# Optimization experiments

Measured on AMD Instinct MI355X. Metric: run time of the kernel, lower is better.

Reference implementation:

```python
import jax, jax.numpy as jnp
import numpy as np

B, S, D, H = 4, 2048, 1024, 16
DH = D // H


def setup_inputs() -> dict:
    key = jax.random.key(0)
    ks = jax.random.split(key, 12)
    std = 0.02
    return {
        "inputs": jax.random.normal(ks[0], (B, S, D), jnp.float32),
        "pre_block": jax.random.normal(ks[1], (B, S, D), jnp.float32),
        "ln_gamma": jnp.ones((D,), jnp.float32),
        "ln_beta": jnp.zeros((D,), jnp.float32),
        "Wq": jax.random.normal(ks[2], (D, D), jnp.float32) * std,
        "bq": jnp.zeros((D,), jnp.float32),
        "Wk": jax.random.normal(ks[3], (D, D), jnp.float32) * std,
        "bk": jnp.zeros((D,), jnp.float32),
        "Wv": jax.random.normal(ks[4], (D, D), jnp.float32) * std,
        "bv": jnp.zeros((D,), jnp.float32),
        "Wpos": jax.random.normal(ks[5], (D, D), jnp.float32) * std,
        "u_bias": jax.random.normal(ks[6], (H, DH), jnp.float32) * std,
        "v_bias": jax.random.normal(ks[7], (H, DH), jnp.float32) * std,
        "Wo": jax.random.normal(ks[8], (D, D), jnp.float32) * std,
        "bo": jnp.zeros((D,), jnp.float32),
    }


def _sinusoidal_pe(seq_len, d_model, dtype):
    pos = jnp.arange(seq_len, dtype=dtype)[:, None]                 # [S,1]
    i = jnp.arange(0, d_model, 2, dtype=dtype)
    div = jnp.exp(-(jnp.log(jnp.asarray(10000.0, dtype)) * i / d_model))  # [D/2]
    ang = pos * div                                                  # [S,D/2]
    pe = jnp.zeros((seq_len, d_model), dtype)
    pe = pe.at[:, 0::2].set(jnp.sin(ang)).at[:, 1::2].set(jnp.cos(ang))
    return pe


def _rel_shift(pos_score):
    # Transformer-XL style relative shift: pos_score [B,H,S,S]
    b, h, s1, s2 = pos_score.shape
    pad = jnp.zeros((b, h, s1, 1), pos_score.dtype)
    padded = jnp.concatenate([pad, pos_score], axis=-1)              # [B,H,S,S+1]
    padded = padded.reshape(b, h, s2 + 1, s1)
    return padded[:, :, 1:].reshape(b, h, s1, s2)


def _layer_norm(x, gamma, beta, eps=1e-5):
    mu = jnp.mean(x, axis=-1, keepdims=True)
    var = jnp.mean(jnp.square(x - mu), axis=-1, keepdims=True)
    return (x - mu) * jax.lax.rsqrt(var + eps) * gamma + beta


def reference(inputs, pre_block, ln_gamma, ln_beta, Wq, bq, Wk, bk, Wv, bv,
              Wpos, u_bias, v_bias, Wo, bo):
    b, s, d = inputs.shape
    h = u_bias.shape[0]
    dh = d // h

    pe = _sinusoidal_pe(s, d, inputs.dtype)                          # [S,D]
    x = _layer_norm(inputs, ln_gamma, ln_beta)

    q = (x @ Wq + bq).reshape(b, s, h, dh)
    k = (x @ Wk + bk).reshape(b, s, h, dh)
    v = (pre_block @ Wv + bv).reshape(b, s, h, dh)
    p = (pe @ Wpos).reshape(s, h, dh)                                # shared across batch

    content = jnp.einsum('bshd,bthd->bhst', q + u_bias, k)           # [B,H,S,S]
    pos_score = jnp.einsum('bshd,thd->bhst', q + v_bias, p)          # [B,H,S,S]
    pos_score = _rel_shift(pos_score)

    score = (content + pos_score) / jnp.sqrt(jnp.asarray(d, inputs.dtype))
    attn = jax.nn.softmax(score, axis=-1)
    ctx = jnp.einsum('bhst,bthd->bshd', attn, v).reshape(b, s, d)
    return ctx @ Wo + bo
```

## Files before the change

### kernel.cpp

```cpp
#include <hip/hip_runtime.h>
#include <hip/hip_bf16.h>
#include <cmath>

#define B_ 4
#define S_ 2048
#define D_ 1024
#define H_ 16
#define DH_ 64

typedef __attribute__((ext_vector_type(8))) short short8;
typedef __attribute__((ext_vector_type(4))) float f32x4;
#define MFMA_BF16(a, b, c) __builtin_amdgcn_mfma_f32_16x16x32_bf16(a, b, c, 0, 0, 0)

static __device__ __forceinline__ float b2f(unsigned short u) {
  union { unsigned int i; float f; } x; x.i = ((unsigned int)u) << 16; return x.f;
}
static __device__ __forceinline__ unsigned short f2b(float f) {
  union { float f; unsigned int i; } x; x.f = f;
  unsigned int r = x.i + 0x7FFFu + ((x.i >> 16) & 1u);
  return (unsigned short)(r >> 16);
}
static __device__ __forceinline__ unsigned int pk2(float a, float b) {
  __hip_bfloat162 h = __float22bfloat162_rn(make_float2(a, b));
  return *(unsigned int*)&h;
}
static __device__ __forceinline__ int mod96(int x) {
  int t = x >> 5;
  int q = (t * 43691) >> 17;
  int m3 = t - q * 3;
  return (x & 31) + (m3 << 5);
}
typedef __attribute__((address_space(3))) unsigned int lds_u32_t;
typedef __attribute__((address_space(1))) const unsigned int glb_u32_t;
static __device__ __forceinline__ void gload_lds16(const void* g, void* l) {
  __builtin_amdgcn_global_load_lds((glb_u32_t*)g, (lds_u32_t*)l, 16, 0, 0);
}

__global__ __launch_bounds__(256) void ln_kernel(const float* __restrict__ in,
                                                 const float* __restrict__ gamma,
                                                 const float* __restrict__ beta,
                                                 unsigned short* __restrict__ out) {
  int row = blockIdx.x;
  const float4* r4 = (const float4*)(in + (size_t)row * D_);
  float4 val = r4[threadIdx.x];
  float s = val.x + val.y + val.z + val.w;
  float sq = val.x * val.x + val.y * val.y + val.z * val.z + val.w * val.w;
#pragma unroll
  for (int o = 32; o > 0; o >>= 1) {
    s += __shfl_down(s, o);
    sq += __shfl_down(sq, o);
  }
  __shared__ float wsum[4], wsq[4];
  __shared__ float smu, srs;
  int wid = threadIdx.x >> 6;
  if ((threadIdx.x & 63) == 0) { wsum[wid] = s; wsq[wid] = sq; }
  __syncthreads();
  if (threadIdx.x == 0) {
    float ts = wsum[0] + wsum[1] + wsum[2] + wsum[3];
    float tq = wsq[0] + wsq[1] + wsq[2] + wsq[3];
    float mu = ts * (1.0f / D_);
    float var = tq * (1.0f / D_) - mu * mu;
    smu = mu;
    srs = rsqrtf(var + 1e-5f);
  }
  __syncthreads();
  float mu = smu, rs = srs;
  float4 g = ((const float4*)gamma)[threadIdx.x];
  float4 be = ((const float4*)beta)[threadIdx.x];
  ushort4 o;
  o.x = f2b((val.x - mu) * rs * g.x + be.x);
  o.y = f2b((val.y - mu) * rs * g.y + be.y);
  o.z = f2b((val.z - mu) * rs * g.z + be.z);
  o.w = f2b((val.w - mu) * rs * g.w + be.w);
  *(ushort4*)(out + (size_t)row * D_ + threadIdx.x * 4) = o;
}

__global__ __launch_bounds__(256) void cast_kernel(const float* __restrict__ in,
                                                   unsigned short* __restrict__ out) {
  size_t idx = (size_t)(blockIdx.x * 256 + threadIdx.x) * 4;
  float4 v = *(const float4*)(in + idx);
  ushort4 o; o.x = f2b(v.x); o.y = f2b(v.y); o.z = f2b(v.z); o.w = f2b(v.w);
  *(ushort4*)(out + idx) = o;
}

__global__ __launch_bounds__(256) void divtab_kernel(double* __restrict__ dt) {
  int i = blockIdx.x * 256 + threadIdx.x;
  dt[i] = exp(-(log(10000.0) * (2.0 * i) / (double)D_));
}

__global__ __launch_bounds__(256) void pe_kernel(const double* __restrict__ dt,
                                                 unsigned short* __restrict__ pe) {
  int idx = blockIdx.x * 256 + threadIdx.x;
  int t = idx >> 9;
  int i = idx & 511;
  double ang = (double)t * dt[i];
  double k = floor(ang * 0.15915494309189535);
  float red = (float)(ang - k * 6.283185307179586);
  ushort2 sc;
  sc.x = f2b(sinf(red));
  sc.y = f2b(cosf(red));
  *(ushort2*)(pe + (size_t)t * D_ + 2 * i) = sc;
}

__global__ __launch_bounds__(256) void wtrans_kernel(const float* __restrict__ W,
                                                     unsigned short* __restrict__ WT) {
  __shared__ float t[64][65];
  int k0 = blockIdx.y * 64, n0 = blockIdx.x * 64;
  int tid = threadIdx.x;
#pragma unroll
  for (int c = 0; c < 4; c++) {
    int idx = tid + c * 256;
    int r = idx >> 4;
    int ch = (idx & 15) * 4;
    float4 d = *(const float4*)(W + (size_t)(k0 + r) * D_ + n0 + ch);
    t[r][ch] = d.x; t[r][ch + 1] = d.y; t[r][ch + 2] = d.z; t[r][ch + 3] = d.w;
  }
  __syncthreads();
  {
    int n = tid >> 2;
    int ch = (tid & 3) * 16;
    unsigned short tmp[8];
#pragma unroll
    for (int half = 0; half < 2; half++) {
#pragma unroll
      for (int e = 0; e < 8; e++) tmp[e] = f2b(t[ch + half * 8 + e][n]);
      *(short8*)(WT + (size_t)(n0 + n) * D_ + k0 + ch + half * 8) = *(short8*)tmp;
    }
  }
}

template <bool F32OUT>
__global__ __launch_bounds__(256) void gemm_bf16_t(const unsigned short* __restrict__ A,
                                                   const unsigned short* __restrict__ BT,
                                                   const float* __restrict__ bias,
                                                   void* __restrict__ Cv,
                                                   int M, int N, int K) {
  __shared__ __align__(16) unsigned short As[128 * 32];
  __shared__ __align__(16) unsigned short Bs[128 * 32];
  const int tid = threadIdx.x;
  const int wid = tid >> 6, lane = tid & 63, quad = lane >> 4, l15 = lane & 15;
  const int m0 = blockIdx.y * 128, n0 = blockIdx.x * 128;
  const int moff = (wid >> 1) * 64, noff = (wid & 1) * 64;
  f32x4 acc[4][4];
#pragma unroll
  for (int i = 0; i < 4; i++)
#pragma unroll
    for (int j = 0; j < 4; j++) acc[i][j] = (f32x4){0.f, 0.f, 0.f, 0.f};

  const int cb0 = wid * 64;
  const int c0 = cb0 + lane;
  const int r0 = c0 >> 2, ch0 = (c0 & 3) * 8;
  const int c1 = c0 + 256;
  const int r1 = c1 >> 2, ch1 = (c1 & 3) * 8;

  for (int k0 = 0; k0 < K; k0 += 32) {
    __syncthreads();
    gload_lds16(A + (size_t)(m0 + r0) * K + k0 + ch0, &As[cb0 * 8]);
    gload_lds16(BT + (size_t)(n0 + r0) * K + k0 + ch0, &Bs[cb0 * 8]);
    gload_lds16(A + (size_t)(m0 + r1) * K + k0 + ch1, &As[(cb0 + 256) * 8]);
    gload_lds16(BT + (size_t)(n0 + r1) * K + k0 + ch1, &Bs[(cb0 + 256) * 8]);
    __syncthreads();
    short8 af[4], bf[4];
#pragma unroll
    for (int i = 0; i < 4; i++)
      af[i] = *(const short8*)&As[(moff + i * 16 + l15) * 32 + quad * 8];
#pragma unroll
    for (int j = 0; j < 4; j++)
      bf[j] = *(const short8*)&Bs[(noff + j * 16 + l15) * 32 + quad * 8];
#pragma unroll
    for (int i = 0; i < 4; i++)
#pragma unroll
      for (int j = 0; j < 4; j++) acc[i][j] = MFMA_BF16(af[i], bf[j], acc[i][j]);
  }
#pragma unroll
  for (int i = 0; i < 4; i++) {
    int row = m0 + moff + i * 16 + quad * 4;
#pragma unroll
    for (int j = 0; j < 4; j++) {
      int col = n0 + noff + j * 16 + l15;
      float bb = bias ? bias[col] : 0.f;
#pragma unroll
      for (int g = 0; g < 4; g++) {
        if (F32OUT)
          ((float*)Cv)[(size_t)(row + g) * N + col] = acc[i][j][g] + bb;
        else
          ((unsigned short*)Cv)[(size_t)(row + g) * N + col] = f2b(acc[i][j][g] + bb);
      }
    }
  }
}

__global__ __launch_bounds__(256) void gemm_qk_bf16(const unsigned short* __restrict__ A,
                                                    const unsigned short* __restrict__ BT,
                                                    const float* __restrict__ bq,
                                                    const float* __restrict__ bk,
                                                    unsigned short* __restrict__ outQ,
                                                    unsigned short* __restrict__ outK) {
  const int K = D_;
  __shared__ __align__(16) unsigned short As[128 * 32];
  __shared__ __align__(16) unsigned short Bs[128 * 32];
  const int tid = threadIdx.x;
  const int wid = tid >> 6, lane = tid & 63, quad = lane >> 4, l15 = lane & 15;
  const int m0 = blockIdx.y * 128, n0 = blockIdx.x * 128;
  const int moff = (wid >> 1) * 64, noff = (wid & 1) * 64;
  f32x4 acc[4][4];
#pragma unroll
  for (int i = 0; i < 4; i++)
#pragma unroll
    for (int j = 0; j < 4; j++) acc[i][j] = (f32x4){0.f, 0.f, 0.f, 0.f};

  const int cb0 = wid * 64;
  const int c0 = cb0 + lane;
  const int r0 = c0 >> 2, ch0 = (c0 & 3) * 8;
  const int c1 = c0 + 256;
  const int r1 = c1 >> 2, ch1 = (c1 & 3) * 8;

  for (int k0 = 0; k0 < K; k0 += 32) {
    __syncthreads();
    gload_lds16(A + (size_t)(m0 + r0) * K + k0 + ch0, &As[cb0 * 8]);
    gload_lds16(BT + (size_t)(n0 + r0) * K + k0 + ch0, &Bs[cb0 * 8]);
    gload_lds16(A + (size_t)(m0 + r1) * K + k0 + ch1, &As[(cb0 + 256) * 8]);
    gload_lds16(BT + (size_t)(n0 + r1) * K + k0 + ch1, &Bs[(cb0 + 256) * 8]);
    __syncthreads();
    short8 af[4], bf[4];
#pragma unroll
    for (int i = 0; i < 4; i++)
      af[i] = *(const short8*)&As[(moff + i * 16 + l15) * 32 + quad * 8];
#pragma unroll
    for (int j = 0; j < 4; j++)
      bf[j] = *(const short8*)&Bs[(noff + j * 16 + l15) * 32 + quad * 8];
#pragma unroll
    for (int i = 0; i < 4; i++)
#pragma unroll
      for (int j = 0; j < 4; j++) acc[i][j] = MFMA_BF16(af[i], bf[j], acc[i][j]);
  }
  const float* bias = (n0 < D_) ? bq : bk;
  unsigned short* outp = (n0 < D_) ? outQ : outK;
  const int nn0 = n0 & (D_ - 1);
#pragma unroll
  for (int i = 0; i < 4; i++) {
    int row = m0 + moff + i * 16 + quad * 4;
#pragma unroll
    for (int j = 0; j < 4; j++) {
      int col = nn0 + noff + j * 16 + l15;
      float bb = bias[col];
#pragma unroll
      for (int g = 0; g < 4; g++)
        outp[(size_t)(row + g) * D_ + col] = f2b(acc[i][j][g] + bb);
    }
  }
}

__global__ __launch_bounds__(256) void vtrans_kernel(const unsigned short* __restrict__ v,
                                                     unsigned short* __restrict__ vt) {
  __shared__ __align__(16) unsigned short t[64 * 72];
  int s0 = blockIdx.x * 64, h = blockIdx.y, b = blockIdx.z;
  int tid = threadIdx.x;
#pragma unroll
  for (int c = 0; c < 2; c++) {
    int idx = tid + c * 256;
    int r = idx >> 3, ch = (idx & 7) * 8;
    short8 d = *(const short8*)(v + (((size_t)b * S_ + s0 + r) * H_ + h) * DH_ + ch);
    *(short8*)&t[r * 72 + ch] = d;
  }
  __syncthreads();
  {
    int dh = tid >> 2, ch = tid & 3;
    unsigned short tmp[8];
#pragma unroll
    for (int half = 0; half < 2; half++) {
#pragma unroll
      for (int e = 0; e < 8; e++) tmp[e] = t[(ch * 16 + half * 8 + e) * 72 + dh];
      *(short8*)(vt + ((size_t)(b * H_ + h) * 64 + dh) * S_ + s0 + ch * 16 + half * 8) =
          *(short8*)tmp;
    }
  }
}

__global__ __launch_bounds__(256) void cw_kernel(const unsigned short* __restrict__ p,
                                                 const float* __restrict__ ub,
                                                 const float* __restrict__ vb,
                                                 float* __restrict__ cw) {
  int idx = blockIdx.x * 256 + threadIdx.x;
  int r = idx & (S_ - 1), h = idx >> 11;
  float s = 0.f;
#pragma unroll 8
  for (int c = 0; c < 64; c++)
    s += (vb[h * 64 + c] - ub[h * 64 + c]) * b2f(p[(size_t)r * D_ + h * 64 + c]);
  cw[idx] = s;
}

__global__ __launch_bounds__(256) void attn_kernel(const unsigned short* __restrict__ q,
                                                   const unsigned short* __restrict__ kg,
                                                   const unsigned short* __restrict__ vtg,
                                                   const unsigned short* __restrict__ pg,
                                                   const float* __restrict__ ub,
                                                   const float* __restrict__ cw,
                                                   unsigned short* __restrict__ ctx) {
  int flat = blockIdx.x + 32 * (blockIdx.y + 16 * blockIdx.z);
  int swz = (flat & 7) * 256 + (flat >> 3);
  const int i0 = (swz & 31) * 64;
  const int h = (swz >> 5) & 15;
  const int b = swz >> 9;
  const int tid = threadIdx.x;
  const int wid = tid >> 6, lane = tid & 63, quad = lane >> 4, l15 = lane & 15;
  const int wr0 = wid * 16;
  const int ib = i0 >> 5;

  __shared__ __align__(16) unsigned short ks[32 * 72];
  __shared__ __align__(16) unsigned short vts[64 * 40];
  __shared__ __align__(16) unsigned short ps[32 * 72];
  __shared__ __align__(16) unsigned short prb[64 * 40];
  __shared__ __align__(16) unsigned short bandA[64 * 99];
  __shared__ __align__(16) unsigned short bandB[64 * 99];

  const int srow = tid >> 3, sch = (tid & 7) * 8;
  const int vrow = tid >> 2, vch = (tid & 3) * 8;

  const unsigned short* kgp = kg + ((size_t)b * S_ * H_ + h) * DH_ + (size_t)srow * H_ * DH_ + sch;
  const unsigned short* vgp = vtg + ((size_t)(b * H_ + h) * 64 + vrow) * S_ + vch;
  const unsigned short* pgp = pg + h * 64 + sch;
  const float* cwh = cw + h * S_;

  short8 qa00, qa01, qa10, qa11;
  {
    auto ldq = [&](int r, int c0) -> short8 {
      int qi = i0 + r; if (qi > S_ - 1) qi = S_ - 1;
      short8 raw = *(const short8*)(q + (((size_t)b * S_ + qi) * H_ + h) * DH_ + c0);
      unsigned short t[8];
#pragma unroll
      for (int e = 0; e < 8; e++)
        t[e] = f2b(b2f((unsigned short)raw[e]) + ub[h * 64 + c0 + e]);
      return *(short8*)t;
    };
    qa00 = ldq(wr0 + l15, quad * 8);
    qa01 = ldq(wr0 + l15, 32 + quad * 8);
    qa10 = ldq(wr0 + l15 + 1, quad * 8);
    qa11 = ldq(wr0 + l15 + 1, 32 + quad * 8);
  }

  auto band_compute = [&](const unsigned short* src, int w, int rhi) {
    int rbase = rhi - 31;
    short8 a0 = w ? qa10 : qa00;
    short8 a1 = w ? qa11 : qa01;
    unsigned short* band = w ? bandB : bandA;
#pragma unroll
    for (int ct = 0; ct < 2; ct++) {
      short8 b0 = *(const short8*)&src[(ct * 16 + l15) * 72 + quad * 8];
      short8 b1 = *(const short8*)&src[(ct * 16 + l15) * 72 + 32 + quad * 8];
      f32x4 acc = (f32x4){0.f, 0.f, 0.f, 0.f};
      acc = MFMA_BF16(a0, b0, acc);
      acc = MFMA_BF16(a1, b1, acc);
      int rr = rbase + ct * 16 + l15;
      int rcl = rr < 0 ? 0 : (rr > S_ - 1 ? S_ - 1 : rr);
      float wv = cwh[rcl];
      int col = mod96(rr + 960);
      int brow0 = wr0 + quad * 4;
      unsigned int v01 = pk2(acc[0] + wv, acc[1] + wv);
      unsigned int v23 = pk2(acc[2] + wv, acc[3] + wv);
      unsigned short e0 = (unsigned short)v01, e1 = (unsigned short)(v01 >> 16);
      unsigned short e2 = (unsigned short)v23, e3 = (unsigned short)(v23 >> 16);
      band[(brow0 + 0) * 99 + col] = e0;
      band[(brow0 + 1) * 99 + col] = e1;
      band[(brow0 + 2) * 99 + col] = e2;
      band[(brow0 + 3) * 99 + col] = e3;
      if (col < 3) {
        band[(brow0 + 0) * 99 + col + 96] = e0;
        band[(brow0 + 1) * 99 + col + 96] = e1;
        band[(brow0 + 2) * 99 + col + 96] = e2;
        band[(brow0 + 3) * 99 + col + 96] = e3;
      }
    }
  };

  {
    int TW[5] = {0, 0, 0, 1, 1};
    int TR[5] = {S_ + 30 - i0 - 64, S_ + 30 - i0 - 32, S_ + 30 - i0, 29, 61};
    for (int t0 = 0; t0 < 5; t0 += 2) {
      if (t0) __syncthreads();
      {
        int rr = TR[t0] - 31 + srow;
        int rc = rr < 0 ? 0 : (rr > S_ - 1 ? S_ - 1 : rr);
        *(short8*)&ps[srow * 72 + sch] = *(const short8*)(pgp + (size_t)rc * D_);
      }
      if (t0 + 1 < 5) {
        int rr = TR[t0 + 1] - 31 + srow;
        int rc = rr < 0 ? 0 : (rr > S_ - 1 ? S_ - 1 : rr);
        *(short8*)&prb[srow * 72 + sch] = *(const short8*)(pgp + (size_t)rc * D_);
      }
      if (t0 == 0) {
        *(short8*)&ks[srow * 72 + sch] = *(const short8*)kgp;
        *(short8*)&vts[vrow * 40 + vch] = *(const short8*)vgp;
      }
      __syncthreads();
      band_compute(ps, TW[t0], TR[t0]);
      if (t0 + 1 < 5) band_compute(prb, TW[t0 + 1], TR[t0 + 1]);
    }
    __syncthreads();
  }

  float lsum = 0.f;
  f32x4 Oa[4];
#pragma unroll
  for (int ct = 0; ct < 4; ct++) Oa[ct] = (f32x4){0.f, 0.f, 0.f, 0.f};

  int cA = mod96(S_ - 1 + quad * 4 - i0 - wr0 - l15);
  int cB = mod96(2112 - 2 + quad * 4 - i0 - wr0 - l15);
  int cwin = 0, crhi = 0, chave = 0;

  const float SCL = 0.03125f;
  const int browA = (wr0 + l15) * 99;
  const unsigned int prbw = (wr0 + l15) * 40 + quad * 4;

  for (int jt = 0; jt < 64; jt++) {
    const int j0 = jt * 32;
    short8 pf_k, pf_v, pf_p;
    int pwin = 0, prhi = 0, havep = 0;
    {
      int j0n = (jt < 63) ? j0 + 32 : j0;
      pf_k = *(const short8*)(kgp + (size_t)j0n * (H_ * DH_));
      pf_v = *(const short8*)(vgp + j0n);
      int j0x = j0 + 32;
      if (j0x <= i0 + 63) { pwin = 0; prhi = S_ + 30 - i0 + j0x; havep = 1; }
      else if (jt < 63)   { pwin = 1; prhi = j0x - i0 + 29;      havep = 1; }
      if (havep) {
        int rr = prhi - 31 + srow;
        int rc = rr < 0 ? 0 : (rr > S_ - 1 ? S_ - 1 : rr);
        pf_p = *(const short8*)(pgp + (size_t)rc * D_);
      }
    }
    if (chave) band_compute(ps, cwin, crhi);
    f32x4 cc[2];
    {
#pragma unroll
      for (int ct = 0; ct < 2; ct++) {
        short8 a0 = *(const short8*)&ks[(ct * 16 + l15) * 72 + quad * 8];
        short8 a1 = *(const short8*)&ks[(ct * 16 + l15) * 72 + 32 + quad * 8];
        f32x4 acc = (f32x4){0.f, 0.f, 0.f, 0.f};
        acc = MFMA_BF16(a0, qa00, acc);
        acc = MFMA_BF16(a1, qa01, acc);
        cc[ct] = acc;
      }
    }
    if (jt < ib) {
#pragma unroll
      for (int ct = 0; ct < 2; ct++) {
        int c0 = ct ? (cA + 16 >= 96 ? cA + 16 - 96 : cA + 16) : cA;
        const unsigned short* base = &bandA[browA + c0];
        float e0 = __expf((cc[ct][0] + b2f(base[0])) * SCL);
        float e1 = __expf((cc[ct][1] + b2f(base[1])) * SCL);
        float e2 = __expf((cc[ct][2] + b2f(base[2])) * SCL);
        float e3 = __expf((cc[ct][3] + b2f(base[3])) * SCL);
        *(uint2*)&prb[prbw + ct * 16] = make_uint2(pk2(e0, e1), pk2(e2, e3));
        lsum += (e0 + e1) + (e2 + e3);
      }
    } else if (jt >= ib + 3) {
#pragma unroll
      for (int ct = 0; ct < 2; ct++) {
        int c0 = ct ? (cB + 16 >= 96 ? cB + 16 - 96 : cB + 16) : cB;
        const unsigned short* base = &bandB[browA + c0];
        float e0 = __expf((cc[ct][0] + b2f(base[0])) * SCL);
        float e1 = __expf((cc[ct][1] + b2f(base[1])) * SCL);
        float e2 = __expf((cc[ct][2] + b2f(base[2])) * SCL);
        float e3 = __expf((cc[ct][3] + b2f(base[3])) * SCL);
        *(uint2*)&prb[prbw + ct * 16] = make_uint2(pk2(e0, e1), pk2(e2, e3));
        lsum += (e0 + e1) + (e2 + e3);
      }
    } else {
#pragma unroll
      for (int ct = 0; ct < 2; ct++) {
        int jbase = j0 + ct * 16 + quad * 4;
        float ev[4];
#pragma unroll
        for (int g = 0; g < 4; g++) {
          int d = jbase + g - (i0 + wr0 + l15);
          float t;
          if (d == 1) t = 0.f;
          else {
            int rr = (d <= 0) ? (S_ - 1 + d) : (d - 2);
            const unsigned short* band = (d <= 0) ? bandA : bandB;
            t = b2f(band[browA + mod96(rr)]);
          }
          ev[g] = __expf((cc[ct][g] + t) * SCL);
          lsum += ev[g];
        }
        *(uint2*)&prb[prbw + ct * 16] = make_uint2(pk2(ev[0], ev[1]), pk2(ev[2], ev[3]));
      }
    }
    {
      short8 af = *(const short8*)&prb[(wr0 + l15) * 40 + quad * 8];
#pragma unroll
      for (int ct = 0; ct < 4; ct++) {
        short8 bf = *(const short8*)&vts[(ct * 16 + l15) * 40 + quad * 8];
        Oa[ct] = MFMA_BF16(af, bf, Oa[ct]);
      }
    }
    __syncthreads();
    *(short8*)&ks[srow * 72 + sch] = pf_k;
    *(short8*)&vts[vrow * 40 + vch] = pf_v;
    if (havep) *(short8*)&ps[srow * 72 + sch] = pf_p;
    cwin = pwin; crhi = prhi; chave = havep;
    __syncthreads();
    cA += 32; if (cA >= 96) cA -= 96;
    cB += 32; if (cB >= 96) cB -= 96;
  }
  float ltot = lsum;
  ltot += __shfl_xor(ltot, 16);
  ltot += __shfl_xor(ltot, 32);
#pragma unroll
  for (int g = 0; g < 4; g++) {
    float lg = __shfl(ltot, quad * 4 + g);
    float inv = 1.f / lg;
    int i = i0 + wr0 + quad * 4 + g;
    unsigned short* dst = ctx + ((size_t)b * S_ + i) * D_ + h * 64;
#pragma unroll
    for (int ct = 0; ct < 4; ct++) dst[ct * 16 + l15] = f2b(Oa[ct][g] * inv);
  }
}

extern "C" void kernel_launch(void* const* d_in, const int* in_sizes, int n_in,
                              void* d_out, int out_size, void* d_ws, size_t ws_size,
                              hipStream_t stream) {
  const float* inputs = (const float*)d_in[0];
  const float* pre_block = (const float*)d_in[1];
  const float* ln_gamma = (const float*)d_in[2];
  const float* ln_beta = (const float*)d_in[3];
  const float* Wq = (const float*)d_in[4];
  const float* bq = (const float*)d_in[5];
  const float* Wk = (const float*)d_in[6];
  const float* bk = (const float*)d_in[7];
  const float* Wv = (const float*)d_in[8];
  const float* bv = (const float*)d_in[9];
  const float* Wpos = (const float*)d_in[10];
  const float* u_bias = (const float*)d_in[11];
  const float* v_bias = (const float*)d_in[12];
  const float* Wo = (const float*)d_in[13];
  const float* bo = (const float*)d_in[14];
  float* out = (float*)d_out;

  char* ws = (char*)d_ws;
  const size_t NBS = (size_t)B_ * S_ * D_;
  unsigned short* xb = (unsigned short*)ws;
  unsigned short* ctx = (unsigned short*)ws;
  unsigned short* preb = (unsigned short*)(ws + NBS * 2);
  unsigned short* peb = (unsigned short*)(ws + NBS * 4);
  char* base = ws + NBS * 4 + (size_t)S_ * D_ * 2;
  unsigned short* wtq = (unsigned short*)(base);
  unsigned short* wtk = (unsigned short*)(base + (size_t)D_ * D_ * 2);
  unsigned short* wtv = (unsigned short*)(base + (size_t)D_ * D_ * 4);
  unsigned short* wtp = (unsigned short*)(base + (size_t)D_ * D_ * 6);
  unsigned short* wto = (unsigned short*)(base + (size_t)D_ * D_ * 8);
  unsigned short* qb = (unsigned short*)(base + (size_t)D_ * D_ * 10);
  unsigned short* kb = qb + NBS;
  unsigned short* vb = kb + NBS;
  unsigned short* vtb = vb + NBS;
  unsigned short* pb = vtb + NBS;
  float* cww = (float*)(pb + (size_t)S_ * D_);
  double* divtab = (double*)wtq;

  ln_kernel<<<B_ * S_, 256, 0, stream>>>(inputs, ln_gamma, ln_beta, xb);
  cast_kernel<<<(int)(NBS / 1024), 256, 0, stream>>>(pre_block, preb);
  divtab_kernel<<<2, 256, 0, stream>>>(divtab);
  pe_kernel<<<(S_ * D_ / 2) / 256, 256, 0, stream>>>(divtab, peb);
  wtrans_kernel<<<dim3(16, 16), 256, 0, stream>>>(Wq, wtq);
  wtrans_kernel<<<dim3(16, 16), 256, 0, stream>>>(Wk, wtk);
  wtrans_kernel<<<dim3(16, 16), 256, 0, stream>>>(Wv, wtv);
  wtrans_kernel<<<dim3(16, 16), 256, 0, stream>>>(Wpos, wtp);
  wtrans_kernel<<<dim3(16, 16), 256, 0, stream>>>(Wo, wto);
  gemm_qk_bf16<<<dim3(16, 64), 256, 0, stream>>>(xb, wtq, bq, bk, qb, kb);
  gemm_bf16_t<false><<<dim3(8, 64), 256, 0, stream>>>(preb, wtv, bv, vb, B_ * S_, D_, D_);
  gemm_bf16_t<false><<<dim3(8, 16), 256, 0, stream>>>(peb, wtp, nullptr, pb, S_, D_, D_);
  vtrans_kernel<<<dim3(32, 16, 4), 256, 0, stream>>>(vb, vtb);
  cw_kernel<<<(H_ * S_) / 256, 256, 0, stream>>>(pb, u_bias, v_bias, cww);
  attn_kernel<<<dim3(32, 16, 4), 256, 0, stream>>>(qb, kb, vtb, pb, u_bias, cww, ctx);
  gemm_bf16_t<true><<<dim3(8, 64), 256, 0, stream>>>(ctx, wto, bo, out, B_ * S_, D_, D_);
}
```

Measured before the change: 644.2 us.

## Merge prep and post kernels, host-compute divtab, and vectorize band stores

```diff
diff --git a/kernel.cpp b/kernel.cpp
--- a/kernel.cpp
+++ b/kernel.cpp
@@ -30,90 +30,102 @@
   int m3 = t - q * 3;
   return (x & 31) + (m3 << 5);
 }
+static __device__ __forceinline__ int clampS(int x) {
+  return x < 0 ? 0 : (x > S_ - 1 ? S_ - 1 : x);
+}
 typedef __attribute__((address_space(3))) unsigned int lds_u32_t;
 typedef __attribute__((address_space(1))) const unsigned int glb_u32_t;
 static __device__ __forceinline__ void gload_lds16(const void* g, void* l) {
   __builtin_amdgcn_global_load_lds((glb_u32_t*)g, (lds_u32_t*)l, 16, 0, 0);
 }
 
-__global__ __launch_bounds__(256) void ln_kernel(const float* __restrict__ in,
-                                                 const float* __restrict__ gamma,
-                                                 const float* __restrict__ beta,
-                                                 unsigned short* __restrict__ out) {
-  int row = blockIdx.x;
-  const float4* r4 = (const float4*)(in + (size_t)row * D_);
-  float4 val = r4[threadIdx.x];
-  float s = val.x + val.y + val.z + val.w;
-  float sq = val.x * val.x + val.y * val.y + val.z * val.z + val.w * val.w;
-#pragma unroll
-  for (int o = 32; o > 0; o >>= 1) {
-    s += __shfl_down(s, o);
-    sq += __shfl_down(sq, o);
-  }
-  __shared__ float wsum[4], wsq[4];
-  __shared__ float smu, srs;
-  int wid = threadIdx.x >> 6;
-  if ((threadIdx.x & 63) == 0) { wsum[wid] = s; wsq[wid] = sq; }
-  __syncthreads();
-  if (threadIdx.x == 0) {
-    float ts = wsum[0] + wsum[1] + wsum[2] + wsum[3];
-    float tq = wsq[0] + wsq[1] + wsq[2] + wsq[3];
-    float mu = ts * (1.0f / D_);
-    float var = tq * (1.0f / D_) - mu * mu;
-    smu = mu;
-    srs = rsqrtf(var + 1e-5f);
-  }
-  __syncthreads();
-  float mu = smu, rs = srs;
-  float4 g = ((const float4*)gamma)[threadIdx.x];
-  float4 be = ((const float4*)beta)[threadIdx.x];
-  ushort4 o;
-  o.x = f2b((val.x - mu) * rs * g.x + be.x);
-  o.y = f2b((val.y - mu) * rs * g.y + be.y);
-  o.z = f2b((val.z - mu) * rs * g.z + be.z);
-  o.w = f2b((val.w - mu) * rs * g.w + be.w);
-  *(ushort4*)(out + (size_t)row * D_ + threadIdx.x * 4) = o;
-}
-
-__global__ __launch_bounds__(256) void cast_kernel(const float* __restrict__ in,
-                                                   unsigned short* __restrict__ out) {
-  size_t idx = (size_t)(blockIdx.x * 256 + threadIdx.x) * 4;
-  float4 v = *(const float4*)(in + idx);
-  ushort4 o; o.x = f2b(v.x); o.y = f2b(v.y); o.z = f2b(v.z); o.w = f2b(v.w);
-  *(ushort4*)(out + idx) = o;
-}
-
-__global__ __launch_bounds__(256) void divtab_kernel(double* __restrict__ dt) {
-  int i = blockIdx.x * 256 + threadIdx.x;
-  dt[i] = exp(-(log(10000.0) * (2.0 * i) / (double)D_));
-}
-
-__global__ __launch_bounds__(256) void pe_kernel(const double* __restrict__ dt,
-                                                 unsigned short* __restrict__ pe) {
-  int idx = blockIdx.x * 256 + threadIdx.x;
-  int t = idx >> 9;
-  int i = idx & 511;
-  double ang = (double)t * dt[i];
-  double k = floor(ang * 0.15915494309189535);
-  float red = (float)(ang - k * 6.283185307179586);
-  ushort2 sc;
-  sc.x = f2b(sinf(red));
-  sc.y = f2b(cosf(red));
-  *(ushort2*)(pe + (size_t)t * D_ + 2 * i) = sc;
-}
-
-__global__ __launch_bounds__(256) void wtrans_kernel(const float* __restrict__ W,
-                                                     unsigned short* __restrict__ WT) {
-  __shared__ float t[64][65];
-  int k0 = blockIdx.y * 64, n0 = blockIdx.x * 64;
+__global__ __launch_bounds__(256) void prep_kernel(
+    const float* __restrict__ inputs, const float* __restrict__ gamma,
+    const float* __restrict__ beta, unsigned short* __restrict__ xb,
+    const float* __restrict__ pre, unsigned short* __restrict__ preb,
+    const double* __restrict__ dt, unsigned short* __restrict__ pe,
+    const float* __restrict__ Wq, unsigned short* __restrict__ wtq,
+    const float* __restrict__ Wk, unsigned short* __restrict__ wtk,
+    const float* __restrict__ Wv, unsigned short* __restrict__ wtv,
+    const float* __restrict__ Wp, unsigned short* __restrict__ wtp,
+    const float* __restrict__ Wo, unsigned short* __restrict__ wto) {
+  __shared__ __align__(16) float shf[64 * 65];
+  int bid = blockIdx.x;
   int tid = threadIdx.x;
+  if (bid < 8192) {
+    int row = bid;
+    float4 val = ((const float4*)(inputs + (size_t)row * D_))[tid];
+    float s = val.x + val.y + val.z + val.w;
+    float sq = val.x * val.x + val.y * val.y + val.z * val.z + val.w * val.w;
+#pragma unroll
+    for (int o = 32; o > 0; o >>= 1) {
+      s += __shfl_down(s, o);
+      sq += __shfl_down(sq, o);
+    }
+    int wid = tid >> 6;
+    if ((tid & 63) == 0) { shf[wid] = s; shf[4 + wid] = sq; }
+    __syncthreads();
+    if (tid == 0) {
+      float ts = shf[0] + shf[1] + shf[2] + shf[3];
+      float tq = shf[4] + shf[5] + shf[6] + shf[7];
+      float mu = ts * (1.0f / D_);
+      float var = tq * (1.0f / D_) - mu * mu;
+      shf[8] = mu;
+      shf[9] = rsqrtf(var + 1e-5f);
+    }
+    __syncthreads();
+    float mu = shf[8], rs = shf[9];
+    float4 g = ((const float4*)gamma)[tid];
+    float4 be = ((const float4*)beta)[tid];
+    ushort4 o;
+    o.x = f2b((val.x - mu) * rs * g.x + be.x);
+    o.y = f2b((val.y - mu) * rs * g.y + be.y);
+    o.z = f2b((val.z - mu) * rs * g.z + be.z);
+    o.w = f2b((val.w - mu) * rs * g.w + be.w);
+    *(ushort4*)(xb + (size_t)row * D_ + tid * 4) = o;
+    return;
+  }
+  bid -= 8192;
+  if (bid < 8192) {
+    size_t idx = (size_t)(bid * 256 + tid) * 4;
+    float4 v = *(const float4*)(pre + idx);
+    ushort4 o; o.x = f2b(v.x); o.y = f2b(v.y); o.z = f2b(v.z); o.w = f2b(v.w);
+    *(ushort4*)(preb + idx) = o;
+    return;
+  }
+  bid -= 8192;
+  if (bid < 4096) {
+    int idx = bid * 256 + tid;
+    int t = idx >> 9;
+    int i = idx & 511;
+    double ang = (double)t * dt[i];
+    double k = floor(ang * 0.15915494309189535);
+    float red = (float)(ang - k * 6.283185307179586);
+    ushort2 sc;
+    sc.x = f2b(sinf(red));
+    sc.y = f2b(cosf(red));
+    *(ushort2*)(pe + (size_t)t * D_ + 2 * i) = sc;
+    return;
+  }
+  bid -= 4096;
+  const float* W; unsigned short* WT;
+  switch (bid >> 8) {
+    case 0: W = Wq; WT = wtq; break;
+    case 1: W = Wk; WT = wtk; break;
+    case 2: W = Wv; WT = wtv; break;
+    case 3: W = Wp; WT = wtp; break;
+    default: W = Wo; WT = wto; break;
+  }
+  int tile = bid & 255;
+  int n0 = (tile & 15) * 64, k0 = (tile >> 4) * 64;
 #pragma unroll
   for (int c = 0; c < 4; c++) {
     int idx = tid + c * 256;
     int r = idx >> 4;
     int ch = (idx & 15) * 4;
     float4 d = *(const float4*)(W + (size_t)(k0 + r) * D_ + n0 + ch);
-    t[r][ch] = d.x; t[r][ch + 1] = d.y; t[r][ch + 2] = d.z; t[r][ch + 3] = d.w;
+    shf[r * 65 + ch] = d.x; shf[r * 65 + ch + 1] = d.y;
+    shf[r * 65 + ch + 2] = d.z; shf[r * 65 + ch + 3] = d.w;
   }
   __syncthreads();
   {
@@ -123,7 +135,7 @@
 #pragma unroll
     for (int half = 0; half < 2; half++) {
 #pragma unroll
-      for (int e = 0; e < 8; e++) tmp[e] = f2b(t[ch + half * 8 + e][n]);
+      for (int e = 0; e < 8; e++) tmp[e] = f2b(shf[(ch + half * 8 + e) * 65 + n]);
       *(short8*)(WT + (size_t)(n0 + n) * D_ + k0 + ch + half * 8) = *(short8*)tmp;
     }
   }
@@ -251,20 +263,25 @@
   }
 }
 
-__global__ __launch_bounds__(256) void vtrans_kernel(const unsigned short* __restrict__ v,
-                                                     unsigned short* __restrict__ vt) {
+__global__ __launch_bounds__(256) void post_kernel(const unsigned short* __restrict__ v,
+                                                   unsigned short* __restrict__ vt,
+                                                   const unsigned short* __restrict__ p,
+                                                   const float* __restrict__ ub,
+                                                   const float* __restrict__ vbb,
+                                                   float* __restrict__ cw) {
   __shared__ __align__(16) unsigned short t[64 * 72];
-  int s0 = blockIdx.x * 64, h = blockIdx.y, b = blockIdx.z;
+  int bid = blockIdx.x;
   int tid = threadIdx.x;
-#pragma unroll
-  for (int c = 0; c < 2; c++) {
-    int idx = tid + c * 256;
-    int r = idx >> 3, ch = (idx & 7) * 8;
-    short8 d = *(const short8*)(v + (((size_t)b * S_ + s0 + r) * H_ + h) * DH_ + ch);
-    *(short8*)&t[r * 72 + ch] = d;
-  }
-  __syncthreads();
-  {
+  if (bid < 2048) {
+    int s0 = (bid & 31) * 64, h = (bid >> 5) & 15, b = bid >> 9;
+#pragma unroll
+    for (int c = 0; c < 2; c++) {
+      int idx = tid + c * 256;
+      int r = idx >> 3, ch = (idx & 7) * 8;
+      short8 d = *(const short8*)(v + (((size_t)b * S_ + s0 + r) * H_ + h) * DH_ + ch);
+      *(short8*)&t[r * 72 + ch] = d;
+    }
+    __syncthreads();
     int dh = tid >> 2, ch = tid & 3;
     unsigned short tmp[8];
 #pragma unroll
@@ -274,19 +291,14 @@
       *(short8*)(vt + ((size_t)(b * H_ + h) * 64 + dh) * S_ + s0 + ch * 16 + half * 8) =
           *(short8*)tmp;
     }
-  }
-}
-
-__global__ __launch_bounds__(256) void cw_kernel(const unsigned short* __restrict__ p,
-                                                 const float* __restrict__ ub,
-                                                 const float* __restrict__ vb,
-                                                 float* __restrict__ cw) {
-  int idx = blockIdx.x * 256 + threadIdx.x;
+    return;
+  }
+  int idx = (bid - 2048) * 256 + tid;
   int r = idx & (S_ - 1), h = idx >> 11;
   float s = 0.f;
 #pragma unroll 8
   for (int c = 0; c < 64; c++)
-    s += (vb[h * 64 + c] - ub[h * 64 + c]) * b2f(p[(size_t)r * D_ + h * 64 + c]);
+    s += (vbb[h * 64 + c] - ub[h * 64 + c]) * b2f(p[(size_t)r * D_ + h * 64 + c]);
   cw[idx] = s;
 }
 
@@ -311,8 +323,8 @@
   __shared__ __align__(16) unsigned short vts[64 * 40];
   __shared__ __align__(16) unsigned short ps[32 * 72];
   __shared__ __align__(16) unsigned short prb[64 * 40];
-  __shared__ __align__(16) unsigned short bandA[64 * 99];
-  __shared__ __align__(16) unsigned short bandB[64 * 99];
+  __shared__ __align__(16) unsigned short bandA[64 * 100];
+  __shared__ __align__(16) unsigned short bandB[64 * 100];
 
   const int srow = tid >> 3, sch = (tid & 7) * 8;
   const int vrow = tid >> 2, vch = (tid & 3) * 8;
@@ -339,37 +351,30 @@
     qa11 = ldq(wr0 + l15 + 1, 32 + quad * 8);
   }
 
+  const int brow = (wr0 + l15) * 100;
+
   auto band_compute = [&](const unsigned short* src, int w, int rhi) {
     int rbase = rhi - 31;
     short8 a0 = w ? qa10 : qa00;
     short8 a1 = w ? qa11 : qa01;
     unsigned short* band = w ? bandB : bandA;
+    const int OFF = w ? 2 : 1;
 #pragma unroll
     for (int ct = 0; ct < 2; ct++) {
       short8 b0 = *(const short8*)&src[(ct * 16 + l15) * 72 + quad * 8];
       short8 b1 = *(const short8*)&src[(ct * 16 + l15) * 72 + 32 + quad * 8];
       f32x4 acc = (f32x4){0.f, 0.f, 0.f, 0.f};
-      acc = MFMA_BF16(a0, b0, acc);
-      acc = MFMA_BF16(a1, b1, acc);
-      int rr = rbase + ct * 16 + l15;
-      int rcl = rr < 0 ? 0 : (rr > S_ - 1 ? S_ - 1 : rr);
-      float wv = cwh[rcl];
-      int col = mod96(rr + 960);
-      int brow0 = wr0 + quad * 4;
-      unsigned int v01 = pk2(acc[0] + wv, acc[1] + wv);
-      unsigned int v23 = pk2(acc[2] + wv, acc[3] + wv);
-      unsigned short e0 = (unsigned short)v01, e1 = (unsigned short)(v01 >> 16);
-      unsigned short e2 = (unsigned short)v23, e3 = (unsigned short)(v23 >> 16);
-      band[(brow0 + 0) * 99 + col] = e0;
-      band[(brow0 + 1) * 99 + col] = e1;
-      band[(brow0 + 2) * 99 + col] = e2;
-      band[(brow0 + 3) * 99 + col] = e3;
-      if (col < 3) {
-        band[(brow0 + 0) * 99 + col + 96] = e0;
-        band[(brow0 + 1) * 99 + col + 96] = e1;
-        band[(brow0 + 2) * 99 + col + 96] = e2;
-        band[(brow0 + 3) * 99 + col + 96] = e3;
-      }
+      acc = MFMA_BF16(b0, a0, acc);
+      acc = MFMA_BF16(b1, a1, acc);
+      int r0 = rbase + ct * 16 + quad * 4;
+      float c0 = cwh[clampS(r0)];
+      float c1 = cwh[clampS(r0 + 1)];
+      float c2 = cwh[clampS(r0 + 2)];
+      float c3 = cwh[clampS(r0 + 3)];
+      int col = mod96(r0 + 960 + OFF);
+      uint2 pv = make_uint2(pk2(acc[0] + c0, acc[1] + c1), pk2(acc[2] + c2, acc[3] + c3));
+      *(uint2*)&band[brow + col] = pv;
+      if (col == 0) *(uint2*)&band[brow + 96] = pv;
     }
   };
 
@@ -380,12 +385,12 @@
       if (t0) __syncthreads();
       {
         int rr = TR[t0] - 31 + srow;
-        int rc = rr < 0 ? 0 : (rr > S_ - 1 ? S_ - 1 : rr);
+        int rc = clampS(rr);
         *(short8*)&ps[srow * 72 + sch] = *(const short8*)(pgp + (size_t)rc * D_);
       }
       if (t0 + 1 < 5) {
         int rr = TR[t0 + 1] - 31 + srow;
-        int rc = rr < 0 ? 0 : (rr > S_ - 1 ? S_ - 1 : rr);
+        int rc = clampS(rr);
         *(short8*)&prb[srow * 72 + sch] = *(const short8*)(pgp + (size_t)rc * D_);
       }
       if (t0 == 0) {
@@ -404,12 +409,11 @@
 #pragma unroll
   for (int ct = 0; ct < 4; ct++) Oa[ct] = (f32x4){0.f, 0.f, 0.f, 0.f};
 
-  int cA = mod96(S_ - 1 + quad * 4 - i0 - wr0 - l15);
-  int cB = mod96(2112 - 2 + quad * 4 - i0 - wr0 - l15);
+  int cA = mod96(S_ + quad * 4 - i0 - wr0 - l15);
+  int cB = mod96(2112 + quad * 4 - i0 - wr0 - l15);
   int cwin = 0, crhi = 0, chave = 0;
 
   const float SCL = 0.03125f;
-  const int browA = (wr0 + l15) * 99;
   const unsigned int prbw = (wr0 + l15) * 40 + quad * 4;
 
   for (int jt = 0; jt < 64; jt++) {
@@ -425,7 +429,7 @@
       else if (jt < 63)   { pwin = 1; prhi = j0x - i0 + 29;      havep = 1; }
       if (havep) {
         int rr = prhi - 31 + srow;
-        int rc = rr < 0 ? 0 : (rr > S_ - 1 ? S_ - 1 : rr);
+        int rc = clampS(rr);
         pf_p = *(const short8*)(pgp + (size_t)rc * D_);
       }
     }
@@ -446,7 +450,7 @@
 #pragma unroll
       for (int ct = 0; ct < 2; ct++) {
         int c0 = ct ? (cA + 16 >= 96 ? cA + 16 - 96 : cA + 16) : cA;
-        const unsigned short* base = &bandA[browA + c0];
+        const unsigned short* base = &bandA[brow + c0];
         float e0 = __expf((cc[ct][0] + b2f(base[0])) * SCL);
         float e1 = __expf((cc[ct][1] + b2f(base[1])) * SCL);
         float e2 = __expf((cc[ct][2] + b2f(base[2])) * SCL);
@@ -458,7 +462,7 @@
 #pragma unroll
       for (int ct = 0; ct < 2; ct++) {
         int c0 = ct ? (cB + 16 >= 96 ? cB + 16 - 96 : cB + 16) : cB;
-        const unsigned short* base = &bandB[browA + c0];
+        const unsigned short* base = &bandB[brow + c0];
         float e0 = __expf((cc[ct][0] + b2f(base[0])) * SCL);
         float e1 = __expf((cc[ct][1] + b2f(base[1])) * SCL);
         float e2 = __expf((cc[ct][2] + b2f(base[2])) * SCL);
@@ -476,11 +480,8 @@
           int d = jbase + g - (i0 + wr0 + l15);
           float t;
           if (d == 1) t = 0.f;
-          else {
-            int rr = (d <= 0) ? (S_ - 1 + d) : (d - 2);
-            const unsigned short* band = (d <= 0) ? bandA : bandB;
-            t = b2f(band[browA + mod96(rr)]);
-          }
+          else if (d <= 0) t = b2f(bandA[brow + mod96(S_ + d)]);
+          else t = b2f(bandB[brow + mod96(d)]);
           ev[g] = __expf((cc[ct][g] + t) * SCL);
           lsum += ev[g];
         }
@@ -556,22 +557,24 @@
   unsigned short* vtb = vb + NBS;
   unsigned short* pb = vtb + NBS;
   float* cww = (float*)(pb + (size_t)S_ * D_);
-  double* divtab = (double*)wtq;
-
-  ln_kernel<<<B_ * S_, 256, 0, stream>>>(inputs, ln_gamma, ln_beta, xb);
-  cast_kernel<<<(int)(NBS / 1024), 256, 0, stream>>>(pre_block, preb);
-  divtab_kernel<<<2, 256, 0, stream>>>(divtab);
-  pe_kernel<<<(S_ * D_ / 2) / 256, 256, 0, stream>>>(divtab, peb);
-  wtrans_kernel<<<dim3(16, 16), 256, 0, stream>>>(Wq, wtq);
-  wtrans_kernel<<<dim3(16, 16), 256, 0, stream>>>(Wk, wtk);
-  wtrans_kernel<<<dim3(16, 16), 256, 0, stream>>>(Wv, wtv);
-  wtrans_kernel<<<dim3(16, 16), 256, 0, stream>>>(Wpos, wtp);
-  wtrans_kernel<<<dim3(16, 16), 256, 0, stream>>>(Wo, wto);
+  double* divtab = (double*)(cww + (size_t)H_ * S_);
+
+  static double h_divtab[512];
+  static bool h_init = false;
+  if (!h_init) {
+    for (int i = 0; i < 512; i++)
+      h_divtab[i] = exp(-(log(10000.0) * (2.0 * i) / (double)D_));
+    h_init = true;
+  }
+  hipMemcpyAsync(divtab, h_divtab, 512 * sizeof(double), hipMemcpyHostToDevice, stream);
+
+  prep_kernel<<<21760, 256, 0, stream>>>(inputs, ln_gamma, ln_beta, xb,
+                                         pre_block, preb, divtab, peb,
+                                         Wq, wtq, Wk, wtk, Wv, wtv, Wpos, wtp, Wo, wto);
   gemm_qk_bf16<<<dim3(16, 64), 256, 0, stream>>>(xb, wtq, bq, bk, qb, kb);
   gemm_bf16_t<false><<<dim3(8, 64), 256, 0, stream>>>(preb, wtv, bv, vb, B_ * S_, D_, D_);
   gemm_bf16_t<false><<<dim3(8, 16), 256, 0, stream>>>(peb, wtp, nullptr, pb, S_, D_, D_);
-  vtrans_kernel<<<dim3(32, 16, 4), 256, 0, stream>>>(vb, vtb);
-  cw_kernel<<<(H_ * S_) / 256, 256, 0, stream>>>(pb, u_bias, v_bias, cww);
+  post_kernel<<<2176, 256, 0, stream>>>(vb, vtb, pb, u_bias, v_bias, cww);
   attn_kernel<<<dim3(32, 16, 4), 256, 0, stream>>>(qb, kb, vtb, pb, u_bias, cww, ctx);
   gemm_bf16_t<true><<<dim3(8, 64), 256, 0, stream>>>(ctx, wto, bo, out, B_ * S_, D_, D_);
 }
```

Measured after the change: 636.0 us. Within noise of the previous version (-1.3%).
